# Performance work log

Hardware: AMD Instinct MI355X
Metric: run time of the kernel (lower is better)

The kernel has to match this reference:

```python
import jax, jax.numpy as jnp
import numpy as np

B, H, T, K = 4, 32, 2048, 64
V = K


def setup_inputs() -> dict:
    key = jax.random.key(0)
    k1, k2, k3, k4, k5 = jax.random.split(key, 5)
    r = jax.random.normal(k1, (B, H, T, K), dtype=jnp.float32)
    k = jax.random.normal(k2, (B, H, T, K), dtype=jnp.float32)
    v = jax.random.normal(k3, (B, H, T, V), dtype=jnp.float32)
    # w is a log-decay; keep it negative so exp(w) in (0,1) and the T-step
    # recurrence is stable (matches real RWKV-6 decay values)
    w = -2.0 * jax.random.uniform(k4, (B, H, T, K), dtype=jnp.float32)
    u = jax.random.normal(k5, (H, K), dtype=jnp.float32)
    initial_state = jnp.zeros((B, H, K, V), dtype=jnp.float32)
    return {"r": r, "k": k, "v": v, "w": w, "u": u, "initial_state": initial_state}


def _rwkv6_scan(r, k, v, w, u, initial_state):
    scale = 1.0
    q = r * scale
    decay = jnp.exp(w)  # [B,H,T,K], matches torch: b_w = exp(w)

    # time-major for scan: [T,B,H,K]
    qT = jnp.moveaxis(q, 2, 0)
    kT = jnp.moveaxis(k, 2, 0)
    vT = jnp.moveaxis(v, 2, 0)
    wT = jnp.moveaxis(decay, 2, 0)

    u_b = u[None, :, :, None]  # [1,H,K,1] broadcast like torch b_u

    def step(h, inp):
        bq, bk, bv, bw = inp  # each [B,H,K] (bv is [B,H,V])
        kv = bk[..., :, None] * bv[..., None, :]          # [B,H,K,V]
        o = jnp.einsum('bhkv,bhk->bhv', h + kv * u_b, bq)  # sum over K
        h = h * bw[..., None] + kv                         # decay-gated update
        return h, o

    final_state, oT = jax.lax.scan(step, initial_state, (qT, kT, vT, wT))
    o = jnp.moveaxis(oT, 0, 2)  # [B,H,T,V]
    return o, final_state


def reference(r, k, v, w, u, initial_state):
    return _rwkv6_scan(r, k, v, w, u, initial_state)
```

## Files before the change

kernel.cpp:

```cpp
#include <hip/hip_runtime.h>
#include <math.h>


#define Bdim 4
#define Hdim 32
#define Tdim 2048
#define Kdim 64
#define Vdim 64
#define NC   32
#define CL   64
#define LP   72

typedef __attribute__((ext_vector_type(8))) short short8;
typedef __attribute__((ext_vector_type(4))) short short4_;
typedef __attribute__((ext_vector_type(4))) float float4_;

__device__ __forceinline__ short f2bf(float x) {
    unsigned u = __float_as_uint(x);
    unsigned r = (u + 0x7FFFu + ((u >> 16) & 1u)) >> 16;
    return (short)r;
}

#define MFMA(a, b, c) __builtin_amdgcn_mfma_f32_16x16x32_bf16(a, b, c, 0, 0, 0)

__device__ __forceinline__ void wg_barrier() {
    __builtin_amdgcn_sched_barrier(0);
    asm volatile("s_waitcnt lgkmcnt(0)");
    __builtin_amdgcn_s_barrier();
    __builtin_amdgcn_sched_barrier(0);
}

__global__ __launch_bounds__(512) void rwkv6_fused(
    const float* __restrict__ rin, const float* __restrict__ kin,
    const float* __restrict__ vin, const float* __restrict__ win,
    const float* __restrict__ uin, const float* __restrict__ init,
    float* __restrict__ oout, float* __restrict__ fin)
{
    __shared__ __attribute__((aligned(16))) short Qh[2][CL * LP];
    __shared__ __attribute__((aligned(16))) short Kh[CL * LP];
    __shared__ __attribute__((aligned(16))) short KhT[2][CL * LP];
    __shared__ __attribute__((aligned(16))) short Am[CL * LP];
    __shared__ __attribute__((aligned(16))) short Vt[2][32 * LP];
    __shared__ __attribute__((aligned(16))) short Ht[2][32 * LP];
    __shared__ float bsum[2][8 * 64];
    __shared__ float Dd[CL];

    const int tid  = threadIdx.x;
    const int wv   = tid >> 6;
    const int lane = tid & 63;
    const int quad = lane >> 4, r = lane & 15;

    const int bid = blockIdx.x;
    const int vh  = bid >> 7;
    const int bh  = bid & 127;
    const int h_idx = bh & (Hdim - 1);

    const int m_s = wv >> 2;
    const int n_s = wv & 3;
    const int k_  = 16 * n_s + r;
    const int i_o = wv >> 1;
    const int n_o = wv & 1;

    const float u_ = uin[h_idx * Kdim + lane];

    const int svrow = tid & 31;
    const int skq   = tid >> 5;

    for (int i = tid; i < CL * LP; i += 512) Am[i] = 0;

    float wl[8], ql[8], kl[8], vls[4];

    auto do_prefetch = [&](size_t nb) {
#pragma unroll
        for (int tt = 0; tt < 8; ++tt) wl[tt] = win[nb + (8 * wv + tt) * Kdim + lane];
#pragma unroll
        for (int i = 0; i < 4; ++i)
            vls[i] = vin[nb + (4 * skq + i) * Kdim + 32 * vh + svrow];
#pragma unroll
        for (int tt = 0; tt < 8; ++tt) ql[tt] = rin[nb + (8 * wv + tt) * Kdim + lane];
#pragma unroll
        for (int tt = 0; tt < 8; ++tt) kl[tt] = kin[nb + (8 * wv + tt) * Kdim + lane];
    };

    auto do_pass1 = [&](int Y) {
        float cwl = 0.f;
#pragma unroll
        for (int tt = 0; tt < 8; ++tt) cwl += wl[tt];
        bsum[Y][wv * 64 + lane] = cwl;
        short4_ pack;
#pragma unroll
        for (int i = 0; i < 4; ++i) pack[i] = f2bf(vls[i]);
        *(short4_*)&Vt[Y][svrow * LP + 4 * skq] = pack;
    };

    auto do_pass2 = [&](int Y) {
        float b8[8];
#pragma unroll
        for (int j = 0; j < 8; ++j) b8[j] = bsum[Y][j * 64 + lane];
        float pref = 0.f;
#pragma unroll
        for (int j = 0; j < 8; ++j) if (j < wv) pref += b8[j];
        const float Cmid = b8[0] + b8[1] + b8[2] + b8[3];
        float cwrun = pref;
        short8 khrow;
        float d3p[8];
#pragma unroll
        for (int tt = 0; tt < 8; ++tt) {
            const int t = 8 * wv + tt;
            const float cwp = cwrun;
            cwrun += wl[tt];
            Qh[Y][t * LP + lane] = f2bf(ql[tt] * __expf(cwp - Cmid));
            const short kv = f2bf(kl[tt] * __expf(Cmid - cwrun));
            Kh[t * LP + lane] = kv;
            khrow[tt] = kv;
            d3p[tt] = ql[tt] * u_ * kl[tt];
        }
        *(short8*)&KhT[Y][lane * LP + wv * 8] = khrow;
#pragma unroll
        for (int off = 32; off > 0; off >>= 1) {
#pragma unroll
            for (int tt = 0; tt < 8; ++tt) d3p[tt] += __shfl_xor(d3p[tt], off);
        }
        if (lane == 0) {
#pragma unroll
            for (int tt = 0; tt < 8; ++tt) Dd[8 * wv + tt] = d3p[tt];
        }
    };

    auto atile = [&](int X, int i, int j) {
        const int trow = 16 * i + r;
        short8 qa0 = *(const short8*)&Qh[X][trow * LP + quad * 8];
        short8 qa1 = *(const short8*)&Qh[X][trow * LP + 32 + quad * 8];
        const int srow = 16 * j + r;
        short8 kb0 = *(const short8*)&Kh[srow * LP + quad * 8];
        short8 kb1 = *(const short8*)&Kh[srow * LP + 32 + quad * 8];
        float4_ acc = {0.f, 0.f, 0.f, 0.f};
        acc = MFMA(qa0, kb0, acc);
        acc = MFMA(qa1, kb1, acc);
#pragma unroll
        for (int reg = 0; reg < 4; ++reg) {
            const int tg = 16 * i + quad * 4 + reg;
            const float val = (tg > srow) ? acc[reg] : ((tg == srow) ? Dd[tg] : 0.f);
            Am[tg * LP + srow] = f2bf(val);
        }
    };

    const size_t bh_base = (size_t)bh * Tdim * Kdim;
    do_prefetch(bh_base);
    do_pass1(0);
    wg_barrier();
    do_pass2(0);
    float h[4];
    {
        const float cm0 = bsum[0][0 * 64 + k_] + bsum[0][64 + k_]
                        + bsum[0][128 + k_] + bsum[0][192 + k_];
        const float eH = __expf(cm0);
#pragma unroll
        for (int reg = 0; reg < 4; ++reg) {
            const int vloc = 16 * m_s + quad * 4 + reg;
            h[reg] = init[((size_t)bh * Kdim + k_) * Vdim + 32 * vh + vloc];
            Ht[0][vloc * LP + k_] = f2bf(h[reg] * eH);
        }
    }
    do_prefetch(bh_base + (size_t)CL * Kdim);
    wg_barrier();

    for (int c = 0; c < NC; ++c) {
        const int X = c & 1, Y = X ^ 1;
        const size_t base = bh_base + (size_t)c * CL * Kdim;

        if (c + 1 < NC) do_pass1(Y);
        __builtin_amdgcn_s_setprio(1);
        {
            int i0, j0;
            if (wv == 0)      { i0 = 0; j0 = 0; }
            else if (wv < 3)  { i0 = 1; j0 = wv - 1; }
            else if (wv < 6)  { i0 = 2; j0 = wv - 3; }
            else              { i0 = 3; j0 = wv - 6; }
            atile(X, i0, j0);
            if (wv < 2) atile(X, 3, 2 + wv);
        }
        __builtin_amdgcn_s_setprio(0);
        wg_barrier();

        if (c + 1 < NC) do_pass2(Y);
        if (c + 2 < NC) do_prefetch(bh_base + (size_t)(c + 2) * CL * Kdim);

        __builtin_amdgcn_s_setprio(1);
        {
            const int trow = 16 * i_o + r;
            short8 aa0 = *(const short8*)&Am[trow * LP + quad * 8];
            short8 aa1 = *(const short8*)&Am[trow * LP + 32 + quad * 8];
            short8 qh0 = *(const short8*)&Qh[X][trow * LP + quad * 8];
            short8 qh1 = *(const short8*)&Qh[X][trow * LP + 32 + quad * 8];
            const int vrow = 16 * n_o + r;
            short8 vb0 = *(const short8*)&Vt[X][vrow * LP + quad * 8];
            short8 vb1 = *(const short8*)&Vt[X][vrow * LP + 32 + quad * 8];
            short8 hb0 = *(const short8*)&Ht[X][vrow * LP + quad * 8];
            short8 hb1 = *(const short8*)&Ht[X][vrow * LP + 32 + quad * 8];
            float4_ o4 = {0.f, 0.f, 0.f, 0.f};
            o4 = MFMA(aa0, vb0, o4);
            o4 = MFMA(aa1, vb1, o4);
            o4 = MFMA(qh0, hb0, o4);
            o4 = MFMA(qh1, hb1, o4);
            float* op = oout + base;
#pragma unroll
            for (int reg = 0; reg < 4; ++reg)
                op[(16 * i_o + quad * 4 + reg) * Vdim + 32 * vh + 16 * n_o + r] = o4[reg];
        }
        float4_ sc = {0.f, 0.f, 0.f, 0.f};
        {
            const int vrow = 16 * m_s + r;
            short8 va0 = *(const short8*)&Vt[X][vrow * LP + quad * 8];
            short8 va1 = *(const short8*)&Vt[X][vrow * LP + 32 + quad * 8];
            short8 kc0 = *(const short8*)&KhT[X][k_ * LP + quad * 8];
            short8 kc1 = *(const short8*)&KhT[X][k_ * LP + 32 + quad * 8];
            sc = MFMA(va0, kc0, sc);
            sc = MFMA(va1, kc1, sc);
        }
        __builtin_amdgcn_s_setprio(0);

        {
            float totk = 0.f, cmk = 0.f;
#pragma unroll
            for (int j = 0; j < 8; ++j) {
                const float bb = bsum[X][j * 64 + k_];
                totk += bb;
                if (j < 4) cmk += bb;
            }
            const float eA = __expf(totk);
            const float eS = __expf(totk - cmk);
#pragma unroll
            for (int reg = 0; reg < 4; ++reg)
                h[reg] = h[reg] * eA + sc[reg] * eS;
            if (c + 1 < NC) {
                const float cm1 = bsum[Y][0 * 64 + k_] + bsum[Y][64 + k_]
                                + bsum[Y][128 + k_] + bsum[Y][192 + k_];
                const float eH = __expf(cm1);
#pragma unroll
                for (int reg = 0; reg < 4; ++reg)
                    Ht[Y][(16 * m_s + quad * 4 + reg) * LP + k_] = f2bf(h[reg] * eH);
            }
        }
        wg_barrier();
    }

#pragma unroll
    for (int reg = 0; reg < 4; ++reg)
        fin[((size_t)bh * Kdim + k_) * Vdim + 32 * vh + 16 * m_s + quad * 4 + reg] = h[reg];
}

extern "C" void kernel_launch(void* const* d_in, const int* in_sizes, int n_in,
                              void* d_out, int out_size, void* d_ws, size_t ws_size,
                              hipStream_t stream) {
    const float* r    = (const float*)d_in[0];
    const float* k    = (const float*)d_in[1];
    const float* v    = (const float*)d_in[2];
    const float* w    = (const float*)d_in[3];
    const float* u    = (const float*)d_in[4];
    const float* init = (const float*)d_in[5];

    float* o   = (float*)d_out;
    float* fin = o + (size_t)Bdim * Hdim * Tdim * Vdim;

    (void)d_ws; (void)ws_size;
    rwkv6_fused<<<Bdim * Hdim * 2, 512, 0, stream>>>(r, k, v, w, u, init, o, fin);
}
```

Measured before the change: 292.4 us.

## Split time sequence into two parallel halves with state correction kernels

Splits each head's 2048-step recurrence into two halves run by separate blocks, doubling the grid and halving the serial chunk chain. The second half starts from zero state and stores decay-scaled bf16 queries. A fix kernel then adds the mid-state contribution to the second half's outputs, and a final kernel combines the two end states. This trades extra launches, workspace traffic and an output read-modify-write for shorter serial latency and better CU occupancy.

```diff
diff --git a/kernel.cpp b/kernel.cpp
--- a/kernel.cpp
+++ b/kernel.cpp
@@ -7,7 +7,7 @@
 #define Tdim 2048
 #define Kdim 64
 #define Vdim 64
-#define NC   32
+#define NCH  16
 #define CL   64
 #define LP   72
 
@@ -30,11 +30,13 @@
     __builtin_amdgcn_sched_barrier(0);
 }
 
-__global__ __launch_bounds__(512) void rwkv6_fused(
+__global__ __launch_bounds__(512) void rwkv6_halves(
     const float* __restrict__ rin, const float* __restrict__ kin,
     const float* __restrict__ vin, const float* __restrict__ win,
     const float* __restrict__ uin, const float* __restrict__ init,
-    float* __restrict__ oout, float* __restrict__ fin)
+    float* __restrict__ oout,
+    unsigned short* __restrict__ qtg, float* __restrict__ hmid,
+    float* __restrict__ hend, float* __restrict__ sumw)
 {
     __shared__ __attribute__((aligned(16))) short Qh[2][CL * LP];
     __shared__ __attribute__((aligned(16))) short Kh[CL * LP];
@@ -51,7 +53,8 @@
     const int quad = lane >> 4, r = lane & 15;
 
     const int bid = blockIdx.x;
-    const int vh  = bid >> 7;
+    const int g   = bid >> 8;
+    const int vh  = (bid >> 7) & 1;
     const int bh  = bid & 127;
     const int h_idx = bh & (Hdim - 1);
 
@@ -69,6 +72,7 @@
     for (int i = tid; i < CL * LP; i += 512) Am[i] = 0;
 
     float wl[8], ql[8], kl[8], vls[4];
+    float cwacc = 0.f;
 
     auto do_prefetch = [&](size_t nb) {
 #pragma unroll
@@ -93,7 +97,7 @@
         *(short4_*)&Vt[Y][svrow * LP + 4 * skq] = pack;
     };
 
-    auto do_pass2 = [&](int Y) {
+    auto do_pass2 = [&](int Y, int cloc) {
         float b8[8];
 #pragma unroll
         for (int j = 0; j < 8; ++j) b8[j] = bsum[Y][j * 64 + lane];
@@ -101,6 +105,7 @@
 #pragma unroll
         for (int j = 0; j < 8; ++j) if (j < wv) pref += b8[j];
         const float Cmid = b8[0] + b8[1] + b8[2] + b8[3];
+        const float tot  = Cmid + b8[4] + b8[5] + b8[6] + b8[7];
         float cwrun = pref;
         short8 khrow;
         float d3p[8];
@@ -114,7 +119,12 @@
             Kh[t * LP + lane] = kv;
             khrow[tt] = kv;
             d3p[tt] = ql[tt] * u_ * kl[tt];
-        }
+            if (g) {
+                qtg[((size_t)bh * 1024 + (size_t)cloc * CL + t) * Kdim + lane]
+                    = (unsigned short)f2bf(ql[tt] * __expf(cwacc + cwp));
+            }
+        }
+        cwacc += tot;
         *(short8*)&KhT[Y][lane * LP + wv * 8] = khrow;
 #pragma unroll
         for (int off = 32; off > 0; off >>= 1) {
@@ -145,11 +155,11 @@
         }
     };
 
-    const size_t bh_base = (size_t)bh * Tdim * Kdim;
-    do_prefetch(bh_base);
+    const size_t half_base = (size_t)bh * Tdim * Kdim + (size_t)g * (Tdim / 2) * Kdim;
+    do_prefetch(half_base);
     do_pass1(0);
     wg_barrier();
-    do_pass2(0);
+    do_pass2(0, 0);
     float h[4];
     {
         const float cm0 = bsum[0][0 * 64 + k_] + bsum[0][64 + k_]
@@ -158,18 +168,19 @@
 #pragma unroll
         for (int reg = 0; reg < 4; ++reg) {
             const int vloc = 16 * m_s + quad * 4 + reg;
-            h[reg] = init[((size_t)bh * Kdim + k_) * Vdim + 32 * vh + vloc];
+            h[reg] = g ? 0.f
+                       : init[((size_t)bh * Kdim + k_) * Vdim + 32 * vh + vloc];
             Ht[0][vloc * LP + k_] = f2bf(h[reg] * eH);
         }
     }
-    do_prefetch(bh_base + (size_t)CL * Kdim);
+    do_prefetch(half_base + (size_t)CL * Kdim);
     wg_barrier();
 
-    for (int c = 0; c < NC; ++c) {
+    for (int c = 0; c < NCH; ++c) {
         const int X = c & 1, Y = X ^ 1;
-        const size_t base = bh_base + (size_t)c * CL * Kdim;
-
-        if (c + 1 < NC) do_pass1(Y);
+        const size_t base = half_base + (size_t)c * CL * Kdim;
+
+        if (c + 1 < NCH) do_pass1(Y);
         __builtin_amdgcn_s_setprio(1);
         {
             int i0, j0;
@@ -183,8 +194,8 @@
         __builtin_amdgcn_s_setprio(0);
         wg_barrier();
 
-        if (c + 1 < NC) do_pass2(Y);
-        if (c + 2 < NC) do_prefetch(bh_base + (size_t)(c + 2) * CL * Kdim);
+        if (c + 1 < NCH) do_pass2(Y, c + 1);
+        if (c + 2 < NCH) do_prefetch(half_base + (size_t)(c + 2) * CL * Kdim);
 
         __builtin_amdgcn_s_setprio(1);
         {
@@ -233,7 +244,7 @@
 #pragma unroll
             for (int reg = 0; reg < 4; ++reg)
                 h[reg] = h[reg] * eA + sc[reg] * eS;
-            if (c + 1 < NC) {
+            if (c + 1 < NCH) {
                 const float cm1 = bsum[Y][0 * 64 + k_] + bsum[Y][64 + k_]
                                 + bsum[Y][128 + k_] + bsum[Y][192 + k_];
                 const float eH = __expf(cm1);
@@ -245,9 +256,69 @@
         wg_barrier();
     }
 
-#pragma unroll
-    for (int reg = 0; reg < 4; ++reg)
-        fin[((size_t)bh * Kdim + k_) * Vdim + 32 * vh + 16 * m_s + quad * 4 + reg] = h[reg];
+    if (g == 0) {
+#pragma unroll
+        for (int reg = 0; reg < 4; ++reg)
+            hmid[((size_t)bh * 64 + 32 * vh + 16 * m_s + quad * 4 + reg) * 64 + k_] = h[reg];
+    } else {
+#pragma unroll
+        for (int reg = 0; reg < 4; ++reg)
+            hend[((size_t)bh * 64 + 32 * vh + 16 * m_s + quad * 4 + reg) * 64 + k_] = h[reg];
+        if (vh == 0 && wv == 0) sumw[bh * 64 + lane] = cwacc;
+    }
+}
+
+__global__ __launch_bounds__(256) void rwkv6_fix(
+    const unsigned short* __restrict__ qtg, const float* __restrict__ hmid,
+    float* __restrict__ oout)
+{
+    __shared__ __attribute__((aligned(16))) short Hm[64 * LP];
+    const int tid = threadIdx.x;
+    const int wv = tid >> 6, lane = tid & 63;
+    const int quad = lane >> 4, r = lane & 15;
+    const int bid = blockIdx.x;
+    const int bh = bid >> 3, slab = bid & 7;
+
+    const float* hm = hmid + (size_t)bh * 4096;
+    for (int i = tid; i < 4096; i += 256)
+        Hm[(i >> 6) * LP + (i & 63)] = f2bf(hm[i]);
+    __syncthreads();
+
+#pragma unroll
+    for (int ti = 0; ti < 2; ++ti) {
+        const int tl0 = slab * 128 + (wv * 2 + ti) * 16;
+        const unsigned short* qrow = qtg + ((size_t)bh * 1024 + tl0 + r) * Kdim;
+        short8 qa0 = *(const short8*)&qrow[quad * 8];
+        short8 qa1 = *(const short8*)&qrow[32 + quad * 8];
+        float* obase = oout + ((size_t)bh * Tdim + 1024 + tl0) * Vdim;
+#pragma unroll
+        for (int n = 0; n < 4; ++n) {
+            short8 hb0 = *(const short8*)&Hm[(16 * n + r) * LP + quad * 8];
+            short8 hb1 = *(const short8*)&Hm[(16 * n + r) * LP + 32 + quad * 8];
+            float4_ acc;
+#pragma unroll
+            for (int reg = 0; reg < 4; ++reg)
+                acc[reg] = obase[(quad * 4 + reg) * Vdim + 16 * n + r];
+            acc = MFMA(qa0, hb0, acc);
+            acc = MFMA(qa1, hb1, acc);
+#pragma unroll
+            for (int reg = 0; reg < 4; ++reg)
+                obase[(quad * 4 + reg) * Vdim + 16 * n + r] = acc[reg];
+        }
+    }
+}
+
+__global__ __launch_bounds__(256) void rwkv6_fin(
+    const float* __restrict__ hmid, const float* __restrict__ hend,
+    const float* __restrict__ sumw, float* __restrict__ fin)
+{
+    const int bh = blockIdx.x, tid = threadIdx.x;
+    for (int i = tid; i < 4096; i += 256) {
+        const int v = i >> 6, k = i & 63;
+        const float e = __expf(sumw[bh * 64 + k]);
+        fin[((size_t)bh * 64 + k) * 64 + v] =
+            hend[(size_t)bh * 4096 + i] + e * hmid[(size_t)bh * 4096 + i];
+    }
 }
 
 extern "C" void kernel_launch(void* const* d_in, const int* in_sizes, int n_in,
@@ -263,6 +334,14 @@
     float* o   = (float*)d_out;
     float* fin = o + (size_t)Bdim * Hdim * Tdim * Vdim;
 
-    (void)d_ws; (void)ws_size;
-    rwkv6_fused<<<Bdim * Hdim * 2, 512, 0, stream>>>(r, k, v, w, u, init, o, fin);
-}
+    unsigned short* qtg = (unsigned short*)d_ws;
+    const size_t QT_ELEMS = (size_t)Bdim * Hdim * (Tdim / 2) * Kdim;
+    float* hmid = (float*)(qtg + QT_ELEMS);
+    float* hend = hmid + (size_t)Bdim * Hdim * Kdim * Vdim;
+    float* sumw = hend + (size_t)Bdim * Hdim * Kdim * Vdim;
+
+    rwkv6_halves<<<512, 512, 0, stream>>>(r, k, v, w, u, init, o,
+                                          qtg, hmid, hend, sumw);
+    rwkv6_fix<<<1024, 256, 0, stream>>>(qtg, hmid, o);
+    rwkv6_fin<<<128, 256, 0, stream>>>(hmid, hend, sumw, fin);
+}
```

Result: slower. 314.4 us (+7.5%).
